# Optimization experiments

Measured on AMD Instinct MI355X. Metric: run time of the kernel, lower is better.

## Reference

```python
import jax, jax.numpy as jnp
import numpy as np

E, T, IN, OUT, GS = 8, 2048, 2048, 2048, 64


def setup_inputs() -> dict:
    key = jax.random.key(0)
    k1, k2, k3, k4, k5 = jax.random.split(key, 5)
    x = jax.random.normal(k1, (T, IN), dtype=jnp.float32)
    # int4 codes in [0,16): stored unpacked as int32 for the reference
    qweight = jax.random.randint(k2, (E, IN, OUT), 0, 16, dtype=jnp.int32)
    G = IN // GS  # quant groups along the reduction dim
    scales = jax.random.uniform(k3, (E, G, OUT), jnp.float32, minval=0.005, maxval=0.02)
    zeros = jax.random.normal(k4, (E, G, OUT), jnp.float32) * 0.01
    scales_and_zeros = jnp.stack([scales, zeros], axis=-1)  # [E, G, OUT, 2]
    # tokens sorted by expert: per-expert counts are diffs of sorted cut points, sum == T
    cuts = jnp.sort(jax.random.randint(k5, (E - 1,), 0, T + 1, dtype=jnp.int32))
    bounds = jnp.concatenate([jnp.zeros((1,), jnp.int32), cuts, jnp.full((1,), T, jnp.int32)])
    tokens_per_expert = jnp.diff(bounds).astype(jnp.int32)  # [E]
    return {
        "x": x,
        "qweight": qweight,
        "scales_and_zeros": scales_and_zeros,
        "tokens_per_expert": tokens_per_expert,
        "group_size": GS,
    }


def reference(x, qweight, scales_and_zeros, tokens_per_expert, group_size):
    """Grouped (per-expert) int4 dequant + GEMM over an expert-sorted token matrix.

    Math of aten._weight_int4pack_mm per expert e over each quant group g:
        W_e[k, n] = (q_e[k, n] - 8) * scale_e[g, n] + zero_e[g, n],  g = k // group_size
        out[rows_e] = x[rows_e] @ W_e
    where rows_e is the contiguous slice given by cumsum(tokens_per_expert).
    """
    n_exp, in_f, out_f = qweight.shape
    n_tok = x.shape[0]
    G = in_f // group_size

    # dequantize all expert weights: [E, IN, OUT]
    q = qweight.reshape(n_exp, G, group_size, out_f).astype(x.dtype)
    scales = scales_and_zeros[..., 0][:, :, None, :]  # [E, G, 1, OUT]
    zeros = scales_and_zeros[..., 1][:, :, None, :]   # [E, G, 1, OUT]
    W = ((q - 8.0) * scales + zeros).reshape(n_exp, in_f, out_f)

    # expert id per token from the cumsum boundaries (tokens are expert-sorted)
    cum = jnp.cumsum(tokens_per_expert)                                # [E]
    eid = jnp.searchsorted(cum, jnp.arange(n_tok), side="right")       # [T]
    onehot = (eid[:, None] == jnp.arange(n_exp)[None, :]).astype(x.dtype)  # [T, E]

    # dispatch -> per-expert GEMM -> combine (jit-safe grouped GEMM)
    xe = jnp.einsum("te,ti->eti", onehot, x)       # [E, T, IN]
    ye = jnp.einsum("eti,eio->eto", xe, W)         # [E, T, OUT]
    out = jnp.einsum("te,eto->to", onehot, ye)     # [T, OUT]
    return out
```

## Files before the change

### kernel.cpp

```cpp
#include <hip/hip_runtime.h>
#include <hip/hip_bf16.h>

constexpr int NE  = 8;
constexpr int T   = 2048;
constexpr int IN  = 2048;
constexpr int OUT = 2048;
constexpr int GS  = 64;
constexpr int G   = IN / GS;

constexpr int BM = 128;
constexpr int BN = 64;
constexpr int BK = 64;
constexpr int NTILE = IN / BK;
constexpr int LDB = 64;

using short8  = __attribute__((ext_vector_type(8))) short;
using short4v = __attribute__((ext_vector_type(4))) short;
using floatx4 = __attribute__((ext_vector_type(4))) float;
using int4v   = __attribute__((ext_vector_type(4))) int;
using float4v = __attribute__((ext_vector_type(4))) float;

__global__ __launch_bounds__(256)
void cvt_x_bf16(const float* __restrict__ x, __hip_bfloat16* __restrict__ xb) {
    const int i = (blockIdx.x * 256 + threadIdx.x) * 4;
    const float4 v = *(const float4*)(x + i);
    union { unsigned long long u; __hip_bfloat162 h2[2]; } p;
    p.h2[0] = __float22bfloat162_rn(float2{v.x, v.y});
    p.h2[1] = __float22bfloat162_rn(float2{v.z, v.w});
    *(unsigned long long*)(xb + i) = p.u;
}

__global__ __launch_bounds__(256, 3)
void hqq_grouped_gemm(const __hip_bfloat16* __restrict__ xb,
                      const int*   __restrict__ qw,
                      const float* __restrict__ snz,
                      const int*   __restrict__ tpe,
                      float* __restrict__ out) {
    const int tid = threadIdx.x;
    const int e   = blockIdx.z;
    const int tm  = blockIdx.y;
    const int n0  = blockIdx.x * BN;

    int b0 = 0;
#pragma unroll
    for (int i = 0; i < NE; ++i) { int c = tpe[i]; if (i < e) b0 += c; }
    const int b1 = b0 + tpe[e];
    const int row0 = b0 + tm * BM;
    if (row0 >= b1) return;

    __shared__ __hip_bfloat16 Bs[2][BN][LDB];

    floatx4 acc[2][4];
#pragma unroll
    for (int i = 0; i < 2; ++i)
#pragma unroll
        for (int j = 0; j < 4; ++j)
            acc[i][j] = (floatx4){0.f, 0.f, 0.f, 0.f};

    const int n4  = (tid & 15) * 4;
    const int kq4 = (tid >> 4) * 4;
    const int wsz = (tid & 3) << 4;

    const int lane = tid & 63;
    const int wid  = tid >> 6;
    const int wm = wid * 32;
    const int lm = lane & 15;
    const int lk = (lane >> 4) * 8;
    const int rsz = ((lm >> 2) & 3) << 4;

    const int*    qbase  = qw + (size_t)e * IN * OUT + n0 + n4;
    const float2* szbase = (const float2*)snz + (size_t)e * G * OUT + n0 + n4;

    const int r0c = min(row0 + wm + lm,      b1 - 1);
    const int r1c = min(row0 + wm + 16 + lm, b1 - 1);
    const __hip_bfloat16* ap0 = xb + (size_t)r0c * IN + lk;
    const __hip_bfloat16* ap1 = xb + (size_t)r1c * IN + lk;

    int4v   qvA[4], qvB[4];
    float4v szA[2], szB[2];
    short8  afA[4], afB[4];

    auto issue_q = [&](int t, int4v (&qv)[4], float4v (&sz)[2]) {
        const int k0 = t * BK;
        const float4v* szp = (const float4v*)(szbase + (size_t)(k0 >> 6) * OUT);
        sz[0] = szp[0];
        sz[1] = szp[1];
#pragma unroll
        for (int kk = 0; kk < 4; ++kk)
            qv[kk] = *(const int4v*)(qbase + (size_t)(k0 + kq4 + kk) * OUT);
    };

    auto issue_af = [&](int t, short8 (&af)[4]) {
        const int k0 = t * BK;
        af[0] = *(const short8*)(ap0 + k0);
        af[1] = *(const short8*)(ap1 + k0);
        af[2] = *(const short8*)(ap0 + k0 + 32);
        af[3] = *(const short8*)(ap1 + k0 + 32);
    };

    auto stage = [&](__hip_bfloat16 (&B)[BN][LDB], int4v (&qv)[4], float4v (&sz)[2]) {
#pragma unroll
        for (int nn = 0; nn < 4; ++nn) {
            const float sc = sz[nn >> 1][(nn & 1) * 2];
            const float cc = sz[nn >> 1][(nn & 1) * 2 + 1] - 8.0f * sc;
            union { short4v v; __hip_bfloat162 h2[2]; } pb;
            pb.h2[0] = __float22bfloat162_rn(float2{(float)qv[0][nn] * sc + cc,
                                                    (float)qv[1][nn] * sc + cc});
            pb.h2[1] = __float22bfloat162_rn(float2{(float)qv[2][nn] * sc + cc,
                                                    (float)qv[3][nn] * sc + cc});
            *(short4v*)&B[n4 + nn][kq4 ^ wsz] = pb.v;
        }
    };

    auto mfma_tile = [&](const __hip_bfloat16 (&B)[BN][LDB], const short8 (&af)[4]) {
#pragma unroll
        for (int ks2 = 0; ks2 < 2; ++ks2) {
            short8 bfr[4];
#pragma unroll
            for (int j = 0; j < 4; ++j)
                bfr[j] = *(const short8*)&B[j * 16 + lm][(ks2 * 32 + lk) ^ rsz];
#pragma unroll
            for (int i = 0; i < 2; ++i)
#pragma unroll
                for (int j = 0; j < 4; ++j)
                    acc[i][j] = __builtin_amdgcn_mfma_f32_16x16x32_bf16(
                        af[ks2 * 2 + i], bfr[j], acc[i][j], 0, 0, 0);
        }
    };

#define TILE_SYNC()                                          \
    asm volatile("s_waitcnt lgkmcnt(0)" ::: "memory");       \
    __builtin_amdgcn_s_barrier();                            \
    __builtin_amdgcn_sched_barrier(0)

    issue_q(0, qvA, szA);
    issue_q(1, qvB, szB);
    issue_af(0, afA);
    issue_af(1, afB);

    for (int t = 0; t < NTILE; t += 2) {
        stage(Bs[0], qvA, szA);
        { const int tn = (t + 2 < NTILE) ? t + 2 : NTILE - 1; issue_q(tn, qvA, szA); }
        TILE_SYNC();
        mfma_tile(Bs[0], afA);
        { const int tn = (t + 2 < NTILE) ? t + 2 : NTILE - 1; issue_af(tn, afA); }

        stage(Bs[1], qvB, szB);
        { const int tn = (t + 3 < NTILE) ? t + 3 : NTILE - 1; issue_q(tn, qvB, szB); }
        TILE_SYNC();
        mfma_tile(Bs[1], afB);
        { const int tn = (t + 3 < NTILE) ? t + 3 : NTILE - 1; issue_af(tn, afB); }
    }
#undef TILE_SYNC

    const int lq = (lane >> 4) * 4;
#pragma unroll
    for (int i = 0; i < 2; ++i) {
#pragma unroll
        for (int r = 0; r < 4; ++r) {
            const int row = row0 + wm + i * 16 + lq + r;
            if (row < b1) {
                float* op = out + (size_t)row * OUT + n0 + lm;
#pragma unroll
                for (int j = 0; j < 4; ++j)
                    op[j * 16] = acc[i][j][r];
            }
        }
    }
}

extern "C" void kernel_launch(void* const* d_in, const int* in_sizes, int n_in,
                              void* d_out, int out_size, void* d_ws, size_t ws_size,
                              hipStream_t stream) {
    const float* x   = (const float*)d_in[0];
    const int*   qw  = (const int*)d_in[1];
    const float* snz = (const float*)d_in[2];
    const int*   tpe = (const int*)d_in[3];
    float* out = (float*)d_out;
    __hip_bfloat16* xb = (__hip_bfloat16*)d_ws;

    cvt_x_bf16<<<(T * IN) / (256 * 4), 256, 0, stream>>>(x, xb);

    dim3 grid(OUT / BN, T / BM, NE);
    hqq_grouped_gemm<<<grid, 256, 0, stream>>>(xb, qw, snz, tpe, out);
}
```

Baseline: 254.6 us.

## Split the K dimension four ways and reduce partial sums with atomics

Each expert/row/column tile is now split into four K-chunks along the reduction dimension, each handled by its own block, which quadruples the grid's z dimension. Partial results are combined with float atomicAdd into an output that is zeroed by a memset first. The aim is more concurrent blocks so the memory-bound weight streaming can hide more latency; occupancy is also raised to 4 blocks per SIMD. In exchange it adds atomic traffic on every output element, an extra memset, and non-deterministic summation order.

```diff
diff --git a/kernel.cpp b/kernel.cpp
--- a/kernel.cpp
+++ b/kernel.cpp
@@ -11,7 +11,9 @@
 constexpr int BM = 128;
 constexpr int BN = 64;
 constexpr int BK = 64;
-constexpr int NTILE = IN / BK;
+constexpr int KSPLIT = 4;
+constexpr int KCH = IN / KSPLIT;
+constexpr int NT  = KCH / BK;
 constexpr int LDB = 64;
 
 using short8  = __attribute__((ext_vector_type(8))) short;
@@ -30,14 +32,15 @@
     *(unsigned long long*)(xb + i) = p.u;
 }
 
-__global__ __launch_bounds__(256, 3)
+__global__ __launch_bounds__(256, 4)
 void hqq_grouped_gemm(const __hip_bfloat16* __restrict__ xb,
                       const int*   __restrict__ qw,
                       const float* __restrict__ snz,
                       const int*   __restrict__ tpe,
                       float* __restrict__ out) {
     const int tid = threadIdx.x;
-    const int e   = blockIdx.z;
+    const int e   = blockIdx.z >> 2;
+    const int kc  = blockIdx.z & 3;
     const int tm  = blockIdx.y;
     const int n0  = blockIdx.x * BN;
 
@@ -133,23 +136,26 @@
     __builtin_amdgcn_s_barrier();                            \
     __builtin_amdgcn_sched_barrier(0)
 
-    issue_q(0, qvA, szA);
-    issue_q(1, qvB, szB);
-    issue_af(0, afA);
-    issue_af(1, afB);
+    const int t0 = kc * NT;
+    const int tL = t0 + NT - 1;
 
-    for (int t = 0; t < NTILE; t += 2) {
+    issue_q(t0,     qvA, szA);
+    issue_q(t0 + 1, qvB, szB);
+    issue_af(t0,     afA);
+    issue_af(t0 + 1, afB);
+
+    for (int t = t0; t < t0 + NT; t += 2) {
         stage(Bs[0], qvA, szA);
-        { const int tn = (t + 2 < NTILE) ? t + 2 : NTILE - 1; issue_q(tn, qvA, szA); }
+        { const int tn = (t + 2 <= tL) ? t + 2 : tL; issue_q(tn, qvA, szA); }
         TILE_SYNC();
         mfma_tile(Bs[0], afA);
-        { const int tn = (t + 2 < NTILE) ? t + 2 : NTILE - 1; issue_af(tn, afA); }
+        { const int tn = (t + 2 <= tL) ? t + 2 : tL; issue_af(tn, afA); }
 
         stage(Bs[1], qvB, szB);
-        { const int tn = (t + 3 < NTILE) ? t + 3 : NTILE - 1; issue_q(tn, qvB, szB); }
+        { const int tn = (t + 3 <= tL) ? t + 3 : tL; issue_q(tn, qvB, szB); }
         TILE_SYNC();
         mfma_tile(Bs[1], afB);
-        { const int tn = (t + 3 < NTILE) ? t + 3 : NTILE - 1; issue_af(tn, afB); }
+        { const int tn = (t + 3 <= tL) ? t + 3 : tL; issue_af(tn, afB); }
     }
 #undef TILE_SYNC
 
@@ -163,7 +169,7 @@
                 float* op = out + (size_t)row * OUT + n0 + lm;
 #pragma unroll
                 for (int j = 0; j < 4; ++j)
-                    op[j * 16] = acc[i][j][r];
+                    atomicAdd(op + j * 16, acc[i][j][r]);
             }
         }
     }
@@ -179,8 +185,10 @@
     float* out = (float*)d_out;
     __hip_bfloat16* xb = (__hip_bfloat16*)d_ws;
 
+    hipMemsetAsync(out, 0, (size_t)out_size * sizeof(float), stream);
+
     cvt_x_bf16<<<(T * IN) / (256 * 4), 256, 0, stream>>>(x, xb);
 
-    dim3 grid(OUT / BN, T / BM, NE);
+    dim3 grid(OUT / BN, T / BM, NE * KSPLIT);
     hqq_grouped_gemm<<<grid, 256, 0, stream>>>(xb, qw, snz, tpe, out);
 }
```

New measurement: 372.3 us. +46.3%, slower.
